# Kernel tuning notes

Hardware: AMD Instinct MI355X
Metric: run time of the kernel (lower is better)

The kernel has to match this reference:

```python
import jax, jax.numpy as jnp
import numpy as np

N = 100000
E = 800000
IN_CH = 128
HID = 32
HEADS = 8
OUT_CH = 40
NEG_SLOPE = 0.2


def setup_inputs() -> dict:
    key = jax.random.key(0)
    ks = jax.random.split(key, 10)
    x = jax.random.normal(ks[0], (N, IN_CH), dtype=jnp.float32)
    edge_index = jax.random.randint(ks[1], (2, E), 0, N, dtype=jnp.int64)
    # GATConv layer 1: in -> heads*hid, concat=True
    s1 = 1.0 / np.sqrt(IN_CH)
    W1 = jax.random.uniform(ks[2], (IN_CH, HEADS * HID), jnp.float32, -s1, s1)
    att_src1 = jax.random.uniform(ks[3], (1, HEADS, HID), jnp.float32, -s1, s1)
    att_dst1 = jax.random.uniform(ks[4], (1, HEADS, HID), jnp.float32, -s1, s1)
    b1 = jnp.zeros((HEADS * HID,), jnp.float32)
    # GATConv layer 2: heads*hid -> out, heads=1, concat=True
    s2 = 1.0 / np.sqrt(HEADS * HID)
    W2 = jax.random.uniform(ks[5], (HEADS * HID, OUT_CH), jnp.float32, -s2, s2)
    att_src2 = jax.random.uniform(ks[6], (1, 1, OUT_CH), jnp.float32, -s2, s2)
    att_dst2 = jax.random.uniform(ks[7], (1, 1, OUT_CH), jnp.float32, -s2, s2)
    b2 = jnp.zeros((OUT_CH,), jnp.float32)
    return {"x": x, "edge_index": edge_index,
            "W1": W1, "att_src1": att_src1, "att_dst1": att_dst1, "b1": b1,
            "W2": W2, "att_src2": att_src2, "att_dst2": att_dst2, "b2": b2}


def _gat_layer(x, src, dst, W, att_src, att_dst, bias, heads, out_ch):
    n = x.shape[0]
    xp = (x @ W).reshape(n, heads, out_ch)               # [N,H,C]
    a_src = jnp.sum(xp * att_src, axis=-1)               # [N,H]
    a_dst = jnp.sum(xp * att_dst, axis=-1)               # [N,H]
    logits = a_src[src] + a_dst[dst]                      # [Etot,H]
    logits = jnp.where(logits > 0, logits, NEG_SLOPE * logits)  # leaky_relu
    # segment softmax over destination node
    m = jax.ops.segment_max(logits, dst, num_segments=n)  # [N,H]
    p = jnp.exp(logits - m[dst])
    z = jax.ops.segment_sum(p, dst, num_segments=n)
    alpha = p / (z[dst] + 1e-16)                           # [Etot,H]
    out = jax.ops.segment_sum(xp[src] * alpha[:, :, None], dst, num_segments=n)
    return out.reshape(n, heads * out_ch) + bias


def reference(x, edge_index, W1, att_src1, att_dst1, b1, W2, att_src2, att_dst2, b2):
    n = x.shape[0]
    # add self loops (PyG GATConv default add_self_loops=True)
    loop = jnp.arange(n, dtype=edge_index.dtype)
    src = jnp.concatenate([edge_index[0], loop])
    dst = jnp.concatenate([edge_index[1], loop])
    # dropout p=0.2 is identity in eval mode
    h = _gat_layer(x, src, dst, W1, att_src1, att_dst1, b1, HEADS, HID)
    h = jax.nn.relu(h)
    out = _gat_layer(h, src, dst, W2, att_src2, att_dst2, b2, 1, OUT_CH)
    return jax.nn.log_softmax(out, axis=1)
```

## Files before the change

### kernel.cpp

```cpp
#include <hip/hip_runtime.h>
#include <math.h>

#define NN 100000
#define NE 800000
#define C1 256
#define OC 40
#define XPAD 64
#define NEG 0.2f
#define FCHUNK 4096
#define G1BLK 1563

typedef _Float16 h4 __attribute__((ext_vector_type(4)));
typedef _Float16 h8 __attribute__((ext_vector_type(8)));
typedef float f4v __attribute__((ext_vector_type(4)));
typedef float f2v __attribute__((ext_vector_type(2)));

static __device__ __forceinline__ float leaky(float v){ return v > 0.f ? v : NEG*v; }

static __device__ __forceinline__ h8 mk8(float4 a, float4 b){
  h8 r = {(_Float16)a.x,(_Float16)a.y,(_Float16)a.z,(_Float16)a.w,
          (_Float16)b.x,(_Float16)b.y,(_Float16)b.z,(_Float16)b.w};
  return r;
}


__global__ __launch_bounds__(256) void k_wt(const float* __restrict__ W1, const float* __restrict__ W2,
                                            const float* __restrict__ aS1, const float* __restrict__ aD1,
                                            const float* __restrict__ aS2, const float* __restrict__ aD2,
                                            _Float16* __restrict__ W1t, _Float16* __restrict__ W2t,
                                            int* __restrict__ deg){
  int b = blockIdx.x;
  if (b < 128){
    int k = b, nb = threadIdx.x;
    W1t[(size_t)nb*128 + k] = (_Float16)W1[k*256 + nb];
  } else if (b < 176){
    int nb = b - 128;
    int e = threadIdx.x;
    int l = e >> 2, j = e & 3;
    int k = (l>>5)*128 + ((l>>4)&1)*64 + j*16 + (l&15);
    float v = (nb < OC) ? W2[(size_t)k*OC + nb] : 0.f;
    W2t[(size_t)nb*256 + e] = (_Float16)v;
  } else if (b < 178){
    int b2 = b - 176;
    int h  = threadIdx.x >> 5;
    int kb = (threadIdx.x & 31) * 4;
    const float* att = b2 ? aD1 : aS1;
    #pragma unroll
    for (int kk = 0; kk < 4; ++kk){
      int k = kb + kk;
      float s = 0.f;
      for (int c = 0; c < 32; ++c) s += W1[k*256 + h*32 + c] * att[h*32 + c];
      W1t[(size_t)(256 + b2*8 + h)*128 + k] = (_Float16)s;
    }
  } else if (b < 194){
    int j = b - 178;
    int e = threadIdx.x;
    int l = e >> 2, jj = e & 3;
    int k = (l>>5)*128 + ((l>>4)&1)*64 + jj*16 + (l&15);
    float v = 0.f;
    if (j == 0){ for (int c = 0; c < OC; ++c) v += W2[(size_t)k*OC + c] * aS2[c]; }
    else if (j == 1){ for (int c = 0; c < OC; ++c) v += W2[(size_t)k*OC + c] * aD2[c]; }
    W2t[(size_t)(48 + j)*256 + e] = (_Float16)v;
  } else {
    int i = (b - 194)*256 + threadIdx.x;
    if (i < NN) deg[i] = 1;
  }
}

__global__ __launch_bounds__(256) void k_gemm1(const float* __restrict__ x,
    const _Float16* __restrict__ W1t, unsigned* __restrict__ xp1w,
    float* __restrict__ asrc, float* __restrict__ adst,
    const int* __restrict__ ei, int* __restrict__ deg)
{
  if (blockIdx.x >= G1BLK){
    int i = (blockIdx.x - G1BLK)*256 + threadIdx.x;
    if (i < NE) atomicAdd(&deg[ei[NE + i]], 1);
    return;
  }
  const int tid  = threadIdx.x;
  const int lane = tid & 63;
  const int w    = tid >> 6;
  const int n = lane & 15, quad = lane >> 4;
  const int r0 = blockIdx.x * 64 + w*16;

  int ra = r0 + n; ra = ra < NN ? ra : NN-1;
  const float* xr = x + (size_t)ra*128 + quad*8;

  float4 fa[4][2];
  #pragma unroll
  for (int ks = 0; ks < 4; ++ks){
    fa[ks][0] = *(const float4*)(xr + ks*32);
    fa[ks][1] = *(const float4*)(xr + ks*32 + 4);
  }

  f4v acc[17];
  #pragma unroll
  for (int ct = 0; ct < 17; ++ct) acc[ct] = (f4v){0.f,0.f,0.f,0.f};

  #pragma unroll
  for (int ks = 0; ks < 4; ++ks){
    h8 a = mk8(fa[ks][0], fa[ks][1]);
    #pragma unroll
    for (int ct = 0; ct < 17; ++ct){
      const int col = (ct < 16) ? (ct*16 + n) : (256 + n);
      h8 b = *(const h8*)(W1t + (size_t)col*128 + ks*32 + quad*8);
      acc[ct] = __builtin_amdgcn_mfma_f32_16x16x32_f16(a, b, acc[ct], 0, 0, 0);
    }
  }

  #pragma unroll
  for (int reg = 0; reg < 4; ++reg){
    const int row = r0 + quad*4 + reg;
    if (row < NN){
      float v[16];
      #pragma unroll
      for (int ct = 0; ct < 16; ++ct) v[ct] = acc[ct][reg];
      unsigned dw0 = (unsigned)__builtin_amdgcn_cvt_pk_fp8_f32(v[0], v[1], 0, false);
      dw0 = (unsigned)__builtin_amdgcn_cvt_pk_fp8_f32(v[2], v[3], (int)dw0, true);
      unsigned dw1 = (unsigned)__builtin_amdgcn_cvt_pk_fp8_f32(v[4], v[5], 0, false);
      dw1 = (unsigned)__builtin_amdgcn_cvt_pk_fp8_f32(v[6], v[7], (int)dw1, true);
      unsigned dw2 = (unsigned)__builtin_amdgcn_cvt_pk_fp8_f32(v[8], v[9], 0, false);
      dw2 = (unsigned)__builtin_amdgcn_cvt_pk_fp8_f32(v[10], v[11], (int)dw2, true);
      unsigned dw3 = (unsigned)__builtin_amdgcn_cvt_pk_fp8_f32(v[12], v[13], 0, false);
      dw3 = (unsigned)__builtin_amdgcn_cvt_pk_fp8_f32(v[14], v[15], (int)dw3, true);
      unsigned* xw = xp1w + (size_t)row*64;
      xw[n]      = dw0;
      xw[16 + n] = dw1;
      xw[32 + n] = dw2;
      xw[48 + n] = dw3;
      float vE = acc[16][reg];
      if (n < 8) asrc[row*8 + n] = vE;
      else       adst[row*8 + (n - 8)] = vE;
    }
  }
}

__global__ __launch_bounds__(256) void k_scan1(const int* __restrict__ deg, int* part, int* bsum){
  __shared__ int lds[256];
  const int t = threadIdx.x;
  const int base = blockIdx.x*1024;
  int v[4]; int s = 0;
  #pragma unroll
  for (int i = 0; i < 4; ++i){ int idx = base + t*4 + i; v[i] = (idx < NN) ? deg[idx] : 0; s += v[i]; }
  lds[t] = s; __syncthreads();
  for (int off = 1; off < 256; off <<= 1){
    int xx = (t >= off) ? lds[t-off] : 0;
    __syncthreads();
    lds[t] += xx;
    __syncthreads();
  }
  int excl = lds[t] - s;
  #pragma unroll
  for (int i = 0; i < 4; ++i){ int idx = base + t*4 + i; if (idx < NN) part[idx] = excl; excl += v[i]; }
  if (t == 255) bsum[blockIdx.x] = lds[255];
}
__global__ void k_scan2(const int* __restrict__ bsum, int* boff){
  const int l = threadIdx.x;
  int a = (l      < 98) ? bsum[l]      : 0;
  int b = (64 + l < 98) ? bsum[64 + l] : 0;
  int sa = a, sb = b;
  #pragma unroll
  for (int off = 1; off < 64; off <<= 1){
    int ta = __shfl_up(sa, off, 64);
    int tb = __shfl_up(sb, off, 64);
    if (l >= off){ sa += ta; sb += tb; }
  }
  const int totalA = __shfl(sa, 63, 64);
  if (l      < 98) boff[l]      = sa - a;
  if (64 + l < 98) boff[64 + l] = totalA + sb - b;
}
__global__ __launch_bounds__(256) void k_scan3(const int* __restrict__ part, const int* __restrict__ boff,
                                               int* rowptr, int* cursor){
  int i = blockIdx.x*256 + threadIdx.x;
  if (i < NN){ int v = part[i] + boff[i >> 10]; rowptr[i] = v; cursor[i] = v; }
  if (i == 0) rowptr[NN] = NN + NE;
}
__global__ __launch_bounds__(256) void k_fill(const int* __restrict__ ei, int* cursor, int* __restrict__ esrc){
  const int xcd = blockIdx.x & 7;
  const int base = (blockIdx.x >> 3) * FCHUNK;
  const int lo = xcd * (NN/8), hi = lo + (NN/8);
  const int end = (base + FCHUNK < NE + NN) ? (base + FCHUNK) : (NE + NN);
  for (int i = base + threadIdx.x; i < end; i += 256){
    int s, d;
    if (i < NE){ s = ei[i]; d = ei[NE + i]; } else { s = d = i - NE; }
    if (d >= lo && d < hi){
      int slot = atomicAdd(&cursor[d], 1);
      esrc[slot] = s;
    }
  }
}

template<int B>
static __device__ __forceinline__ void agg1_batch(
    const int j0, const int je, const int lane,
    const int* __restrict__ esrc, const float* __restrict__ asrc,
    const float adA, const float adB,
    const unsigned* __restrict__ xp1w,
    f2v& accLo, f2v& accHi, float& z0, float& z1)
{
  const int cnt = je - j0;
  const int slot = lane & 15;
  const int hA = (lane >> 4) << 1;
  int idx = j0 + slot; idx = idx < je ? idx : je - 1;
  const int sv = esrc[idx];
  float pv0 = 0.f, pv1 = 0.f;
  if (slot < cnt){
    f2v av = *(const f2v*)(asrc + (size_t)sv*8 + hA);
    pv0 = __expf(leaky(av.x + adA));
    pv1 = __expf(leaky(av.y + adB));
  }
  z0 += pv0; z1 += pv1;
  unsigned u[B];
  #pragma unroll
  for (int e = 0; e < B; ++e){
    int s = __builtin_amdgcn_readlane(sv, e);
    u[e] = xp1w[(size_t)s*64 + lane];
  }
  __builtin_amdgcn_sched_barrier(0);
  const int pb = lane & 48;
  #pragma unroll
  for (int e = 0; e < B; ++e){
    const float pA = __shfl(pv0, pb | e, 64);
    const float pB = __shfl(pv1, pb | e, 64);
    f2v lo = __builtin_amdgcn_cvt_pk_f32_fp8((int)u[e], false);
    f2v hi = __builtin_amdgcn_cvt_pk_f32_fp8((int)u[e], true);
    accLo += (f2v){pA, pA} * lo;
    accHi += (f2v){pB, pB} * hi;
  }
}

__global__ __launch_bounds__(256) void k_agg1(const unsigned* __restrict__ xp1w,
    const float* __restrict__ asrc, const float* __restrict__ adst,
    const float* __restrict__ b1, const int* __restrict__ rowptr,
    const int* __restrict__ esrc, _Float16* __restrict__ h1)
{
  const int lane = threadIdx.x & 63;
  int n = __builtin_amdgcn_readfirstlane(blockIdx.x*4 + (threadIdx.x >> 6));
  const int hA = (lane >> 4) << 1;
  const f2v ad = *(const f2v*)(adst + (size_t)n*8 + hA);
  const int jb = rowptr[n], je = rowptr[n+1];
  const int cbase = (lane>>5)*128 + ((lane>>4)&1)*64 + (lane&15);
  const float bp0 = b1[cbase], bp1 = b1[cbase+16], bp2 = b1[cbase+32], bp3 = b1[cbase+48];
  f2v accLo = {0.f,0.f}, accHi = {0.f,0.f};
  float z0 = 0.f, z1 = 0.f;

  int j0 = jb;
  while (j0 < je){
    if (je - j0 > 8){
      agg1_batch<16>(j0, je, lane, esrc, asrc, ad.x, ad.y, xp1w, accLo, accHi, z0, z1);
      j0 += 16;
    } else {
      agg1_batch<8>(j0, je, lane, esrc, asrc, ad.x, ad.y, xp1w, accLo, accHi, z0, z1);
      j0 += 8;
    }
  }
  #pragma unroll
  for (int off = 1; off <= 8; off <<= 1){
    z0 += __shfl_xor(z0, off, 64);
    z1 += __shfl_xor(z1, off, 64);
  }
  const float invA = 1.f/(z0 + 1e-16f), invB = 1.f/(z1 + 1e-16f);
  h4 o = {(_Float16)fmaxf(accLo.x*invA + bp0, 0.f),
          (_Float16)fmaxf(accLo.y*invA + bp1, 0.f),
          (_Float16)fmaxf(accHi.x*invB + bp2, 0.f),
          (_Float16)fmaxf(accHi.y*invB + bp3, 0.f)};
  ((h4*)h1)[(size_t)n*64 + lane] = o;
}

__global__ __launch_bounds__(256) void k_gemm2(const _Float16* __restrict__ h1,
    const _Float16* __restrict__ W2t, _Float16* __restrict__ xp2,
    float* __restrict__ asrc2, float* __restrict__ adst2)
{
  const int tid  = threadIdx.x;
  const int lane = tid & 63;
  const int w    = tid >> 6;
  const int n = lane & 15, quad = lane >> 4;
  const int r0 = blockIdx.x * 64 + w*16;

  f4v acc[4];
  #pragma unroll
  for (int ct = 0; ct < 4; ++ct) acc[ct] = (f4v){0.f,0.f,0.f,0.f};

  int rr = r0 + n; rr = rr < NN ? rr : NN-1;

  #pragma unroll
  for (int ks = 0; ks < 8; ++ks){
    h8 a = *(const h8*)(h1 + (size_t)rr*256 + ks*32 + quad*8);
    #pragma unroll
    for (int ct = 0; ct < 4; ++ct){
      h8 b = *(const h8*)(W2t + (size_t)(ct*16 + n)*256 + ks*32 + quad*8);
      acc[ct] = __builtin_amdgcn_mfma_f32_16x16x32_f16(a, b, acc[ct], 0, 0, 0);
    }
  }

  #pragma unroll
  for (int reg = 0; reg < 4; ++reg){
    const int row = r0 + quad*4 + reg;
    if (row < NN){
      float v0 = acc[0][reg], v1 = acc[1][reg], v2 = acc[2][reg], v3 = acc[3][reg];
      _Float16* xr = xp2 + (size_t)row*XPAD + n;
      xr[0]  = (_Float16)v0;
      xr[16] = (_Float16)v1;
      if (n < 8) xr[32] = (_Float16)v2;
      if (n == 0) asrc2[row] = v3;
      if (n == 1) adst2[row] = v3;
    }
  }
}

__global__ __launch_bounds__(256) void k_agg2(const _Float16* __restrict__ xp2,
    const float* __restrict__ asrc2, const float* __restrict__ adst2,
    const float* __restrict__ b2, const int* __restrict__ rowptr,
    const int* __restrict__ esrc, float* __restrict__ out)
{
  const int lane = threadIdx.x & 63;
  const int g = lane >> 4;
  const int t = lane & 15;
  int n = __builtin_amdgcn_readfirstlane(blockIdx.x*4 + (threadIdx.x >> 6));
  const float ad = adst2[n];
  const int jb = rowptr[n], je = rowptr[n+1];
  f4v acc = {0.f,0.f,0.f,0.f};
  float zacc = 0.f;

  for (int j0 = jb; j0 < je; j0 += 16){
    const int cnt = je - j0;
    int idx = j0 + t; idx = idx < je ? idx : je - 1;
    const int sv = esrc[idx];
    const float pv = (t < cnt) ? __expf(leaky(asrc2[sv] + ad)) : 0.f;
    zacc += pv;
    h4 u[4];
    #pragma unroll
    for (int e4 = 0; e4 < 4; ++e4){
      int svg = __shfl(sv, e4*4 + g, 64);
      u[e4] = *(const h4*)(xp2 + (size_t)svg*XPAD + t*4);
    }
    __builtin_amdgcn_sched_barrier(0);
    #pragma unroll
    for (int e4 = 0; e4 < 4; ++e4){
      const float p = __shfl(pv, e4*4 + g, 64);
      acc.x += p*(float)u[e4].x;
      acc.y += p*(float)u[e4].y;
      acc.z += p*(float)u[e4].z;
      acc.w += p*(float)u[e4].w;
    }
  }
  #pragma unroll
  for (int off = 1; off <= 8; off <<= 1) zacc += __shfl_xor(zacc, off, 64);
  #pragma unroll
  for (int off = 16; off <= 32; off <<= 1){
    acc.x += __shfl_xor(acc.x, off, 64);
    acc.y += __shfl_xor(acc.y, off, 64);
    acc.z += __shfl_xor(acc.z, off, 64);
    acc.w += __shfl_xor(acc.w, off, 64);
  }
  const float inv = 1.f/(zacc + 1e-16f);
  const bool act = t < 10;
  float4 bv = act ? *(const float4*)(b2 + 4*t) : make_float4(0.f,0.f,0.f,0.f);
  float v0 = acc.x*inv + bv.x, v1 = acc.y*inv + bv.y;
  float v2 = acc.z*inv + bv.z, v3 = acc.w*inv + bv.w;
  float m = act ? fmaxf(fmaxf(v0,v1), fmaxf(v2,v3)) : -INFINITY;
  #pragma unroll
  for (int off = 1; off <= 8; off <<= 1) m = fmaxf(m, __shfl_xor(m, off, 64));
  float es = act ? (__expf(v0-m)+__expf(v1-m)+__expf(v2-m)+__expf(v3-m)) : 0.f;
  #pragma unroll
  for (int off = 1; off <= 8; off <<= 1) es += __shfl_xor(es, off, 64);
  if (lane < 10){
    float lse = m + __logf(es);
    float4 o = make_float4(v0-lse, v1-lse, v2-lse, v3-lse);
    *(float4*)(out + (size_t)n*OC + 4*t) = o;
  }
}

extern "C" void kernel_launch(void* const* d_in, const int* in_sizes, int n_in,
                              void* d_out, int out_size, void* d_ws, size_t ws_size,
                              hipStream_t stream)
{
  const float* x   = (const float*)d_in[0];
  const int*   ei  = (const int*)  d_in[1];
  const float* W1  = (const float*)d_in[2];
  const float* aS1 = (const float*)d_in[3];
  const float* aD1 = (const float*)d_in[4];
  const float* b1  = (const float*)d_in[5];
  const float* W2  = (const float*)d_in[6];
  const float* aS2 = (const float*)d_in[7];
  const float* aD2 = (const float*)d_in[8];
  const float* b2  = (const float*)d_in[9];
  float* out = (float*)d_out;

  char* wsp = (char*)d_ws;
  size_t off = 0;
  auto alloc = [&](size_t bytes){ void* p = wsp + off; off += (bytes + 255) & ~(size_t)255; return p; };
  unsigned* xp1w = (unsigned*)alloc((size_t)NN*C1);
  _Float16* h1  = (_Float16*)alloc((size_t)NN*C1*2);
  float* as1  = (float*)alloc((size_t)NN*8*4);
  float* ad1  = (float*)alloc((size_t)NN*8*4);
  float* as2  = (float*)alloc((size_t)NN*4);
  float* ad2  = (float*)alloc((size_t)NN*4);
  int* deg    = (int*)alloc((size_t)NN*4);
  int* part   = (int*)alloc((size_t)NN*4);
  int* rowptr = (int*)alloc((size_t)(NN+1)*4);
  int* cursor = (int*)alloc((size_t)NN*4);
  int* bsum   = (int*)alloc(98*4);
  int* boff   = (int*)alloc(98*4);
  int* esrc   = (int*)alloc((size_t)(NN+NE)*4);
  _Float16* W1t = (_Float16*)alloc((size_t)272*128*2);
  _Float16* W2t = (_Float16*)alloc((size_t)64*256*2);
  _Float16* xp2 = (_Float16*)alloc((size_t)NN*XPAD*2);
  (void)ws_size; (void)in_sizes; (void)n_in; (void)out_size;

  const int fill_chunks = (NE + NN + FCHUNK - 1) / FCHUNK;
  const int deg_blocks  = (NE + 255) / 256;

  k_wt    <<<194 + (NN + 255)/256, 256, 0, stream>>>(W1, W2, aS1, aD1, aS2, aD2, W1t, W2t, deg);
  k_gemm1 <<<G1BLK + deg_blocks,   256, 0, stream>>>(x, W1t, xp1w, as1, ad1, ei, deg);
  k_scan1 <<<98,   256, 0, stream>>>(deg, part, bsum);
  k_scan2 <<<1,    64,  0, stream>>>(bsum, boff);
  k_scan3 <<<391,  256, 0, stream>>>(part, boff, rowptr, cursor);
  k_fill  <<<fill_chunks*8, 256, 0, stream>>>(ei, cursor, esrc);
  k_agg1  <<<25000,256, 0, stream>>>(xp1w, as1, ad1, b1, rowptr, esrc, h1);
  k_gemm2 <<<1563, 256, 0, stream>>>(h1, W2t, xp2, as2, ad2);
  k_agg2  <<<25000,256, 0, stream>>>(xp2, as2, ad2, b2, rowptr, esrc, out);
}
```

Before: 355.6 us.

## Stage swizzled W1 into LDS with 512-thread GEMM1 blocks

GEMM1 now copies the whole 272x128 fp16 weight matrix (W1 plus the attention-projection columns) into shared memory with direct global-to-LDS loads. It stores it in an XOR-swizzled layout so the MFMA B-fragment reads avoid bank conflicts. Blocks grow to 512 threads covering 128 rows, so each LDS copy is reused by more waves. The intent is to replace repeated per-wave global/L2 reads of the weights with LDS reads. In exchange, about 70 KB of LDS per block limits residency, and the degree-counting blocks that share this kernel also reserve that LDS.

```diff
diff --git a/kernel.cpp b/kernel.cpp
--- a/kernel.cpp
+++ b/kernel.cpp
@@ -8,7 +8,7 @@
 #define XPAD 64
 #define NEG 0.2f
 #define FCHUNK 4096
-#define G1BLK 1563
+#define G1BLK 782
 
 typedef _Float16 h4 __attribute__((ext_vector_type(4)));
 typedef _Float16 h8 __attribute__((ext_vector_type(8)));
@@ -23,16 +23,21 @@
   return r;
 }
 
+static __device__ __forceinline__ void gload_lds16h(const _Float16* g, _Float16* l){
+  __builtin_amdgcn_global_load_lds((const __attribute__((address_space(1))) void*)g,
+                                   (__attribute__((address_space(3))) void*)l, 16, 0, 0);
+}
+
 
 __global__ __launch_bounds__(256) void k_wt(const float* __restrict__ W1, const float* __restrict__ W2,
                                             const float* __restrict__ aS1, const float* __restrict__ aD1,
                                             const float* __restrict__ aS2, const float* __restrict__ aD2,
-                                            _Float16* __restrict__ W1t, _Float16* __restrict__ W2t,
+                                            _Float16* __restrict__ W1s, _Float16* __restrict__ W2t,
                                             int* __restrict__ deg){
   int b = blockIdx.x;
   if (b < 128){
-    int k = b, nb = threadIdx.x;
-    W1t[(size_t)nb*128 + k] = (_Float16)W1[k*256 + nb];
+    int k = b, c = threadIdx.x;
+    W1s[(size_t)c*128 + (((k>>3) ^ (c&15))<<3) + (k&7)] = (_Float16)W1[k*256 + c];
   } else if (b < 176){
     int nb = b - 128;
     int e = threadIdx.x;
@@ -45,12 +50,13 @@
     int h  = threadIdx.x >> 5;
     int kb = (threadIdx.x & 31) * 4;
     const float* att = b2 ? aD1 : aS1;
+    const int c = 256 + b2*8 + h;
     #pragma unroll
     for (int kk = 0; kk < 4; ++kk){
       int k = kb + kk;
       float s = 0.f;
-      for (int c = 0; c < 32; ++c) s += W1[k*256 + h*32 + c] * att[h*32 + c];
-      W1t[(size_t)(256 + b2*8 + h)*128 + k] = (_Float16)s;
+      for (int cc = 0; cc < 32; ++cc) s += W1[k*256 + h*32 + cc] * att[h*32 + cc];
+      W1s[(size_t)c*128 + (((k>>3) ^ (c&15))<<3) + (k&7)] = (_Float16)s;
     }
   } else if (b < 194){
     int j = b - 178;
@@ -67,13 +73,14 @@
   }
 }
 
-__global__ __launch_bounds__(256) void k_gemm1(const float* __restrict__ x,
-    const _Float16* __restrict__ W1t, unsigned* __restrict__ xp1w,
+__global__ __launch_bounds__(512, 4) void k_gemm1(const float* __restrict__ x,
+    const _Float16* __restrict__ W1s, unsigned* __restrict__ xp1w,
     float* __restrict__ asrc, float* __restrict__ adst,
     const int* __restrict__ ei, int* __restrict__ deg)
 {
+  __shared__ _Float16 bs[272*128];
   if (blockIdx.x >= G1BLK){
-    int i = (blockIdx.x - G1BLK)*256 + threadIdx.x;
+    int i = (blockIdx.x - G1BLK)*512 + threadIdx.x;
     if (i < NE) atomicAdd(&deg[ei[NE + i]], 1);
     return;
   }
@@ -81,17 +88,28 @@
   const int lane = tid & 63;
   const int w    = tid >> 6;
   const int n = lane & 15, quad = lane >> 4;
-  const int r0 = blockIdx.x * 64 + w*16;
+  const int r0 = blockIdx.x * 128 + w*16;
+
+  #pragma unroll
+  for (int it = 0; it < 8; ++it){
+    int idx = it*512 + tid;
+    gload_lds16h(W1s + (size_t)idx*8, bs + (size_t)(it*512 + w*64)*8);
+  }
+  if (w < 4){
+    int idx = 4096 + w*64 + lane;
+    gload_lds16h(W1s + (size_t)idx*8, bs + (size_t)(4096 + w*64)*8);
+  }
 
   int ra = r0 + n; ra = ra < NN ? ra : NN-1;
   const float* xr = x + (size_t)ra*128 + quad*8;
-
   float4 fa[4][2];
   #pragma unroll
   for (int ks = 0; ks < 4; ++ks){
     fa[ks][0] = *(const float4*)(xr + ks*32);
     fa[ks][1] = *(const float4*)(xr + ks*32 + 4);
   }
+
+  __syncthreads();
 
   f4v acc[17];
   #pragma unroll
@@ -102,8 +120,8 @@
     h8 a = mk8(fa[ks][0], fa[ks][1]);
     #pragma unroll
     for (int ct = 0; ct < 17; ++ct){
-      const int col = (ct < 16) ? (ct*16 + n) : (256 + n);
-      h8 b = *(const h8*)(W1t + (size_t)col*128 + ks*32 + quad*8);
+      const int col = ct*16 + n;
+      h8 b = *((const h8*)bs + (size_t)col*16 + (((ks*4 + quad) ^ n)));
       acc[ct] = __builtin_amdgcn_mfma_f32_16x16x32_f16(a, b, acc[ct], 0, 0, 0);
     }
   }
@@ -403,16 +421,16 @@
   int* bsum   = (int*)alloc(98*4);
   int* boff   = (int*)alloc(98*4);
   int* esrc   = (int*)alloc((size_t)(NN+NE)*4);
-  _Float16* W1t = (_Float16*)alloc((size_t)272*128*2);
+  _Float16* W1s = (_Float16*)alloc((size_t)272*128*2);
   _Float16* W2t = (_Float16*)alloc((size_t)64*256*2);
   _Float16* xp2 = (_Float16*)alloc((size_t)NN*XPAD*2);
   (void)ws_size; (void)in_sizes; (void)n_in; (void)out_size;
 
   const int fill_chunks = (NE + NN + FCHUNK - 1) / FCHUNK;
-  const int deg_blocks  = (NE + 255) / 256;
-
-  k_wt    <<<194 + (NN + 255)/256, 256, 0, stream>>>(W1, W2, aS1, aD1, aS2, aD2, W1t, W2t, deg);
-  k_gemm1 <<<G1BLK + deg_blocks,   256, 0, stream>>>(x, W1t, xp1w, as1, ad1, ei, deg);
+  const int deg_blocks  = (NE + 511) / 512;
+
+  k_wt    <<<194 + (NN + 255)/256, 256, 0, stream>>>(W1, W2, aS1, aD1, aS2, aD2, W1s, W2t, deg);
+  k_gemm1 <<<G1BLK + deg_blocks,   512, 0, stream>>>(x, W1s, xp1w, as1, ad1, ei, deg);
   k_scan1 <<<98,   256, 0, stream>>>(deg, part, bsum);
   k_scan2 <<<1,    64,  0, stream>>>(bsum, boff);
   k_scan3 <<<391,  256, 0, stream>>>(part, boff, rowptr, cursor);
```

Measured after the change: 322.7 us. -9.2%, faster.
